# Optimization experiments

Measured on AMD Instinct MI355X. Metric: run time of the kernel, lower is better.

Reference implementation:

```python
import jax, jax.numpy as jnp
import numpy as np

TOP_K = 4
ALPHA = 1.702
LIMIT = 7.0


def _glu(x):
    # interleaved gate/up split, clamp, custom swiglu
    gate = x[..., ::2]
    up = x[..., 1::2]
    gate = jnp.minimum(gate, LIMIT)
    up = jnp.clip(up, -LIMIT, LIMIT)
    glu = gate * jax.nn.sigmoid(gate * ALPHA)
    return (up + 1.0) * glu


def setup_inputs() -> dict:
    key = jax.random.key(0)
    ks = jax.random.split(key, 7)
    B, S, H, F, E = 1, 1024, 2880, 2880, 16
    w_scale = 0.02
    return {
        "hidden_states": jax.random.normal(ks[0], (B, S, H), dtype=jnp.float32),
        "router_w": jax.random.normal(ks[1], (E, H), dtype=jnp.float32) * w_scale,
        "router_b": jax.random.normal(ks[2], (E,), dtype=jnp.float32) * w_scale,
        "gate_up_w": jax.random.normal(ks[3], (E, H, 2 * F), dtype=jnp.float32) * w_scale,
        "gate_up_b": jax.random.normal(ks[4], (E, 2 * F), dtype=jnp.float32) * w_scale,
        "down_w": jax.random.normal(ks[5], (E, F, H), dtype=jnp.float32) * w_scale,
        "down_b": jax.random.normal(ks[6], (E, H), dtype=jnp.float32) * w_scale,
    }


def reference(hidden_states, router_w, router_b, gate_up_w, gate_up_b, down_w, down_b):
    B, S, H = hidden_states.shape
    x = hidden_states.reshape(-1, H)  # [T, H]
    T = x.shape[0]

    # Router: linear + top-k + softmax over top-k values, scattered to full [T, E]
    logits = x @ router_w.T + router_b  # [T, E]
    top_v, top_i = jax.lax.top_k(logits, TOP_K)  # [T, K]
    top_v = jax.nn.softmax(top_v, axis=-1)  # normalized top-k affinities
    scores = jnp.zeros_like(logits).at[jnp.arange(T)[:, None], top_i].set(top_v)  # [T, E]

    # Expert GLU MLPs (dense over experts; zero affinity masks unselected experts)
    gu = jnp.einsum('th,ehf->etf', x, gate_up_w) + gate_up_b[:, None, :]  # [E, T, 2F]
    act = _glu(gu)  # [E, T, F]
    out_e = jnp.einsum('etf,efh->eth', act, down_w) + down_b[:, None, :]  # [E, T, H]

    # Combine weighted by router scores
    out = jnp.einsum('te,eth->th', scores, out_e)  # [T, H]
    return out.reshape(B, S, H)
```

## Files before the change

kernel.cpp:

```cpp
#include <hip/hip_runtime.h>
#include <hip/hip_bf16.h>
#include <math.h>

#define H_DIM 2880
#define F_DIM 2880
#define GU_DIM 5760
#define NE 16
#define NT 1024
#define TOPK 4
#define NIT 90

typedef float f32x4 __attribute__((ext_vector_type(4)));
typedef __bf16 bf16x8 __attribute__((ext_vector_type(8)));

__device__ __forceinline__ unsigned short f2bf(float f) {
    union { float f; unsigned u; } v; v.f = f;
    return (unsigned short)((v.u + 0x8000u) >> 16);
}
__device__ __forceinline__ unsigned pk2(float a, float b) {
    return (unsigned)f2bf(a) | ((unsigned)f2bf(b) << 16);
}
__device__ __forceinline__ void gload16(const void* gsrc, void* ldst) {
    __builtin_amdgcn_global_load_lds(
        (const __attribute__((address_space(1))) unsigned int*)gsrc,
        (__attribute__((address_space(3))) unsigned int*)ldst,
        16, 0, 0);
}

__global__ __launch_bounds__(256) void castx_kernel(const float* __restrict__ x,
                                                    unsigned short* __restrict__ xb)
{
    int i = (blockIdx.x * 256 + threadIdx.x) * 8;
    float4 a = *(const float4*)(x + i);
    float4 b = *(const float4*)(x + i + 4);
    uint4 o;
    o.x = pk2(a.x, a.y); o.y = pk2(a.z, a.w);
    o.z = pk2(b.x, b.y); o.w = pk2(b.z, b.w);
    *(uint4*)(xb + i) = o;
}

__global__ __launch_bounds__(64) void router_kernel(
    const float* __restrict__ x, const float* __restrict__ rw, const float* __restrict__ rb,
    int* counts, int* topk_idx, float* topk_score)
{
    int t = blockIdx.x, lane = threadIdx.x;
    const float* xr = x + (size_t)t * H_DIM;
    float acc[NE];
#pragma unroll
    for (int e = 0; e < NE; e++) acc[e] = 0.f;
    for (int h = lane; h < H_DIM; h += 64) {
        float xv = xr[h];
#pragma unroll
        for (int e = 0; e < NE; e++) acc[e] += xv * rw[e * H_DIM + h];
    }
    float lg[NE];
#pragma unroll
    for (int e = 0; e < NE; e++) {
        float v = acc[e];
#pragma unroll
        for (int off = 32; off > 0; off >>= 1) v += __shfl_down(v, off, 64);
        lg[e] = v;
    }
    if (lane == 0) {
#pragma unroll
        for (int e = 0; e < NE; e++) lg[e] += rb[e];
        int mask = 0; float tv[TOPK]; int ti[TOPK];
        for (int k = 0; k < TOPK; k++) {
            float best = -1e30f; int bi = 0;
            for (int e = 0; e < NE; e++)
                if (!((mask >> e) & 1) && lg[e] > best) { best = lg[e]; bi = e; }
            mask |= 1 << bi; tv[k] = best; ti[k] = bi;
        }
        float m = tv[0], s = 0.f, ex[TOPK];
        for (int k = 0; k < TOPK; k++) { ex[k] = expf(tv[k] - m); s += ex[k]; }
        float inv = 1.f / s;
        for (int k = 0; k < TOPK; k++) {
            topk_idx[t * TOPK + k] = ti[k];
            topk_score[t * TOPK + k] = ex[k] * inv;
            atomicAdd(&counts[ti[k]], 1);
        }
    }
}

__global__ void offsets_kernel(const int* counts, int* offsets) {
    if (threadIdx.x == 0 && blockIdx.x == 0) {
        int s = 0;
        for (int e = 0; e < NE; e++) { offsets[e] = s; s += counts[e]; }
        offsets[NE] = s;
    }
}

__global__ void scatter_kernel(const int* topk_idx, const float* topk_score,
                               const int* offsets, int* fills, int* entry, float* entry_score,
                               int* slot_map)
{
    int t = blockIdx.x * blockDim.x + threadIdx.x;
    if (t >= NT) return;
    for (int k = 0; k < TOPK; k++) {
        int e = topk_idx[t * TOPK + k];
        int pos = atomicAdd(&fills[e], 1);
        int i = offsets[e] + pos;
        entry[i] = t | (k << 16);
        entry_score[i] = topk_score[t * TOPK + k];
        slot_map[t * TOPK + k] = i;
    }
}


#define PIPE_ISSUE(ASRC0, ASRC1, BPTR, BSTRIDE, KK, NB, RS)                   \
    {                                                                         \
        gload16((ASRC0) + (KK), &As[NB][aoff0]);                              \
        gload16((ASRC1) + (KK), &As[NB][aoff1]);                              \
        RS[0] = *(const float4*)((BPTR) + (size_t)(KK) * (BSTRIDE));          \
        RS[1] = *(const float4*)((BPTR) + (size_t)((KK) + 1) * (BSTRIDE));    \
        asm volatile("" ::: "memory");                                        \
    }

#define PIPE_BWRITE(NB, RC)                                                   \
    {                                                                         \
        float4 t0_ = RC[0], t1_ = RC[1];                                      \
        *(unsigned*)&Bs[NB][bwr0] = pk2(t0_.x, t1_.x);                        \
        *(unsigned*)&Bs[NB][bwr1] = pk2(t0_.y, t1_.y);                        \
        *(unsigned*)&Bs[NB][bwr2] = pk2(t0_.z, t1_.z);                        \
        *(unsigned*)&Bs[NB][bwr3] = pk2(t0_.w, t1_.w);                        \
    }

#define PIPE_BARRIER()                                                        \
    asm volatile("s_waitcnt lgkmcnt(0)" ::: "memory");                        \
    __builtin_amdgcn_sched_barrier(0);                                        \
    __builtin_amdgcn_s_barrier();                                             \
    __builtin_amdgcn_sched_barrier(0);

#define PIPE_MFMA(CUR)                                                        \
    {                                                                         \
        bf16x8 af_[4], bq_[4];                                                \
        _Pragma("unroll") for (int i = 0; i < 4; i++)                         \
            af_[i] = *(const bf16x8*)&As[CUR][a_rd[i]];                       \
        _Pragma("unroll") for (int i = 0; i < 4; i++)                         \
            bq_[i] = *(const bf16x8*)&Bs[CUR][b_rd[i]];                       \
        _Pragma("unroll") for (int mi = 0; mi < 4; mi++)                      \
            _Pragma("unroll") for (int ni = 0; ni < 4; ni++)                  \
                acc[mi][ni] = __builtin_amdgcn_mfma_f32_16x16x32_bf16(        \
                    af_[mi], bq_[ni], acc[mi][ni], 0, 0, 0);                  \
    }

#define PIPE_BODY(ASRC0, ASRC1, BPTR, BSTRIDE, T, CUR, NB1, NB2, RISS, RCON)  \
    {                                                                         \
        bool more_ = (T) + 2 < NIT;                                           \
        if (more_) PIPE_ISSUE(ASRC0, ASRC1, BPTR, BSTRIDE, ((T) + 2) * 32, NB2, RISS); \
        PIPE_MFMA(CUR);                                                       \
        if ((T) + 1 < NIT) {                                                  \
            if (more_) { asm volatile("s_waitcnt vmcnt(4)" ::: "memory"); }   \
            else       { asm volatile("s_waitcnt vmcnt(0)" ::: "memory"); }   \
            PIPE_BWRITE(NB1, RCON);                                           \
            PIPE_BARRIER();                                                   \
        }                                                                     \
    }

__global__ __launch_bounds__(512, 4) void gemm1_kernel(
    const unsigned short* __restrict__ xb, const float* __restrict__ gw, const float* __restrict__ gb,
    const int* __restrict__ counts, const int* __restrict__ offsets,
    const int* __restrict__ entry, unsigned short* __restrict__ act)
{
    int e = blockIdx.z;
    int cnt = counts[e];
    int m0 = blockIdx.y * 256;
    if (m0 >= cnt) return;
    int n0 = blockIdx.x * 128;
    int off = offsets[e];

    __shared__ __align__(16) unsigned short As[3][256 * 32];
    __shared__ __align__(16) unsigned short Bs[3][128 * 40];
    __shared__ int toks[256];

    int tid = threadIdx.x;
    if (tid < 256) {
        int r = m0 + tid;
        toks[tid] = entry[off + (r < cnt ? r : 0)] & 0xFFFF;
    }
    __syncthreads();

    int wv = tid >> 6, lane = tid & 63;

    int ar0 = 32 * wv + (lane >> 2);
    int ar1 = ar0 + 16;
    int ac = lane & 3;
    const unsigned short* asrc0 = xb + (size_t)toks[ar0] * H_DIM + 8 * (ac ^ ((ar0 >> 1) & 3));
    const unsigned short* asrc1 = xb + (size_t)toks[ar1] * H_DIM + 8 * (ac ^ ((ar1 >> 1) & 3));
    int aoff0 = (32 * wv) * 32;
    int aoff1 = (32 * wv + 16) * 32;

    int n4 = tid & 31, ks = tid >> 5;
    const float* bptr = gw + (size_t)e * H_DIM * GU_DIM + (size_t)(ks * 2) * GU_DIM + n0 + n4 * 4;
    int bswz = (((ks >> 2) ^ (n4 & 3)) * 8) + (ks & 3) * 2;
    int bwr0 = (n4 * 4 + 0) * 40 + bswz;
    int bwr1 = (n4 * 4 + 1) * 40 + bswz;
    int bwr2 = (n4 * 4 + 2) * 40 + bswz;
    int bwr3 = (n4 * 4 + 3) * 40 + bswz;

    int wm = (wv >> 1) * 64, wn = (wv & 1) * 64;
    int r16 = lane & 15, q = lane >> 4;

    f32x4 acc[4][4] = {};
    int a_rd[4], b_rd[4];
#pragma unroll
    for (int i = 0; i < 4; i++) {
        int m = wm + i * 16 + r16;
        a_rd[i] = m * 32 + ((q ^ ((m >> 1) & 3)) * 8);
        int n = wn + i * 16 + r16;
        b_rd[i] = n * 40 + ((q ^ ((n >> 2) & 3)) * 8);
    }

    float4 rA[2], rB[2];
    PIPE_ISSUE(asrc0, asrc1, bptr, GU_DIM, 0, 0, rA);
    PIPE_ISSUE(asrc0, asrc1, bptr, GU_DIM, 32, 1, rB);
    asm volatile("s_waitcnt vmcnt(4)" ::: "memory");
    PIPE_BWRITE(0, rA);
    PIPE_BARRIER();

    int c0 = 0;
    for (int it = 0; it < NIT; it += 2) {
        int c1 = c0 + 1; if (c1 == 3) c1 = 0;
        int c2 = c1 + 1; if (c2 == 3) c2 = 0;
        PIPE_BODY(asrc0, asrc1, bptr, GU_DIM, it,     c0, c1, c2, rA, rB);
        PIPE_BODY(asrc0, asrc1, bptr, GU_DIM, it + 1, c1, c2, c0, rB, rA);
        c0 = c2;
    }

    const float* gbp = gb + (size_t)e * GU_DIM;
#pragma unroll
    for (int ni = 0; ni < 4; ni++) {
        int col = n0 + wn + ni * 16 + r16;
        float bias = gbp[col];
#pragma unroll
        for (int mi = 0; mi < 4; mi++) {
#pragma unroll
            for (int r = 0; r < 4; r++) {
                float v = acc[mi][ni][r] + bias;
                float vo = __shfl_xor(v, 1, 64);
                float gate = (lane & 1) ? vo : v;
                float up   = (lane & 1) ? v  : vo;
                gate = fminf(gate, 7.0f);
                up = fminf(fmaxf(up, -7.0f), 7.0f);
                float glu = gate / (1.0f + expf(-1.702f * gate));
                float a = (up + 1.0f) * glu;
                int row = m0 + wm + mi * 16 + q * 4 + r;
                if (row < cnt && !(lane & 1))
                    act[(size_t)(off + row) * F_DIM + (col >> 1)] = f2bf(a);
            }
        }
    }
}

__global__ __launch_bounds__(512, 4) void gemm2_kernel(
    const unsigned short* __restrict__ act, const float* __restrict__ dw, const float* __restrict__ db,
    const int* __restrict__ counts, const int* __restrict__ offsets,
    const float* __restrict__ entry_score, float* __restrict__ slot_out)
{
    int e = blockIdx.z;
    int cnt = counts[e];
    int m0 = blockIdx.y * 256;
    if (m0 >= cnt) return;
    int n0 = blockIdx.x * 128;
    int off = offsets[e];

    __shared__ __align__(16) unsigned short As[3][256 * 32];
    __shared__ __align__(16) unsigned short Bs[3][128 * 40];
    __shared__ float scs[256];

    int tid = threadIdx.x;
    if (tid < 256) {
        int r = m0 + tid;
        scs[tid] = entry_score[off + (r < cnt ? r : 0)];
    }
    __syncthreads();

    int wv = tid >> 6, lane = tid & 63;

    int ar0 = 32 * wv + (lane >> 2);
    int ar1 = ar0 + 16;
    int ac = lane & 3;
    const unsigned short* asrc0 = act + (size_t)(off + m0 + ar0) * F_DIM + 8 * (ac ^ ((ar0 >> 1) & 3));
    const unsigned short* asrc1 = act + (size_t)(off + m0 + ar1) * F_DIM + 8 * (ac ^ ((ar1 >> 1) & 3));
    int aoff0 = (32 * wv) * 32;
    int aoff1 = (32 * wv + 16) * 32;

    int n4 = tid & 31, ks = tid >> 5;
    int ncol = n0 + n4 * 4;
    int ncc = (ncol < H_DIM) ? ncol : (H_DIM - 4);
    const float* bptr = dw + (size_t)e * F_DIM * H_DIM + (size_t)(ks * 2) * H_DIM + ncc;
    int bswz = (((ks >> 2) ^ (n4 & 3)) * 8) + (ks & 3) * 2;
    int bwr0 = (n4 * 4 + 0) * 40 + bswz;
    int bwr1 = (n4 * 4 + 1) * 40 + bswz;
    int bwr2 = (n4 * 4 + 2) * 40 + bswz;
    int bwr3 = (n4 * 4 + 3) * 40 + bswz;

    int wm = (wv >> 1) * 64, wn = (wv & 1) * 64;
    int r16 = lane & 15, q = lane >> 4;

    f32x4 acc[4][4] = {};
    int a_rd[4], b_rd[4];
#pragma unroll
    for (int i = 0; i < 4; i++) {
        int m = wm + i * 16 + r16;
        a_rd[i] = m * 32 + ((q ^ ((m >> 1) & 3)) * 8);
        int n = wn + i * 16 + r16;
        b_rd[i] = n * 40 + ((q ^ ((n >> 2) & 3)) * 8);
    }

    float4 rA[2], rB[2];
    PIPE_ISSUE(asrc0, asrc1, bptr, H_DIM, 0, 0, rA);
    PIPE_ISSUE(asrc0, asrc1, bptr, H_DIM, 32, 1, rB);
    asm volatile("s_waitcnt vmcnt(4)" ::: "memory");
    PIPE_BWRITE(0, rA);
    PIPE_BARRIER();

    int c0 = 0;
    for (int it = 0; it < NIT; it += 2) {
        int c1 = c0 + 1; if (c1 == 3) c1 = 0;
        int c2 = c1 + 1; if (c2 == 3) c2 = 0;
        PIPE_BODY(asrc0, asrc1, bptr, H_DIM, it,     c0, c1, c2, rA, rB);
        PIPE_BODY(asrc0, asrc1, bptr, H_DIM, it + 1, c1, c2, c0, rB, rA);
        c0 = c2;
    }

    const float* dbp = db + (size_t)e * H_DIM;
#pragma unroll
    for (int ni = 0; ni < 4; ni++) {
        int col = n0 + wn + ni * 16 + r16;
        float bias = (col < H_DIM) ? dbp[col] : 0.f;
#pragma unroll
        for (int mi = 0; mi < 4; mi++) {
#pragma unroll
            for (int r = 0; r < 4; r++) {
                int lr = wm + mi * 16 + q * 4 + r;
                if (m0 + lr < cnt && col < H_DIM) {
                    float v = (acc[mi][ni][r] + bias) * scs[lr];
                    slot_out[(size_t)(off + m0 + lr) * H_DIM + col] = v;
                }
            }
        }
    }
}

__global__ __launch_bounds__(256) void gather_kernel(
    const float* __restrict__ slot_out, const int* __restrict__ slot_map,
    float* __restrict__ out)
{
    int t = blockIdx.x;
    int s0 = slot_map[t * TOPK + 0];
    int s1 = slot_map[t * TOPK + 1];
    int s2 = slot_map[t * TOPK + 2];
    int s3 = slot_map[t * TOPK + 3];
    const float* r0 = slot_out + (size_t)s0 * H_DIM;
    const float* r1 = slot_out + (size_t)s1 * H_DIM;
    const float* r2 = slot_out + (size_t)s2 * H_DIM;
    const float* r3 = slot_out + (size_t)s3 * H_DIM;
    float* op = out + (size_t)t * H_DIM;
    for (int h = threadIdx.x * 4; h < H_DIM; h += 1024) {
        f32x4 v = *(const f32x4*)(r0 + h) + *(const f32x4*)(r1 + h)
                + *(const f32x4*)(r2 + h) + *(const f32x4*)(r3 + h);
        *(f32x4*)(op + h) = v;
    }
}

extern "C" void kernel_launch(void* const* d_in, const int* in_sizes, int n_in,
                              void* d_out, int out_size, void* d_ws, size_t ws_size,
                              hipStream_t stream)
{
    const float* x  = (const float*)d_in[0];
    const float* rw = (const float*)d_in[1];
    const float* rb = (const float*)d_in[2];
    const float* gw = (const float*)d_in[3];
    const float* gb = (const float*)d_in[4];
    const float* dw = (const float*)d_in[5];
    const float* db = (const float*)d_in[6];
    float* out = (float*)d_out;

    char* ws = (char*)d_ws;
    int*   counts      = (int*)(ws);
    int*   fills       = (int*)(ws + 64);
    int*   offsets     = (int*)(ws + 128);
    int*   topk_idx    = (int*)(ws + 256);
    float* topk_score  = (float*)(ws + 16640);
    int*   entry       = (int*)(ws + 33024);
    float* entry_score = (float*)(ws + 49408);
    int*   slot_map    = (int*)(ws + 65792);
    unsigned short* act = (unsigned short*)(ws + 131072);
    unsigned short* xb  = (unsigned short*)(ws + 25198592);
    float* slot_out     = (float*)(ws + 31096832);

    hipMemsetAsync(ws, 0, 256, stream);

    castx_kernel<<<1440, 256, 0, stream>>>(x, xb);
    router_kernel<<<NT, 64, 0, stream>>>(x, rw, rb, counts, topk_idx, topk_score);
    offsets_kernel<<<1, 32, 0, stream>>>(counts, offsets);
    scatter_kernel<<<4, 256, 0, stream>>>(topk_idx, topk_score, offsets, fills, entry, entry_score, slot_map);
    gemm1_kernel<<<dim3(45, 4, NE), 512, 0, stream>>>(xb, gw, gb, counts, offsets, entry, act);
    gemm2_kernel<<<dim3(23, 4, NE), 512, 0, stream>>>(act, dw, db, counts, offsets, entry_score, slot_out);
    gather_kernel<<<NT, 256, 0, stream>>>(slot_out, slot_map, out);
}
```

Measured before the change: 2.126 ms.

## Widen GEMM tiles to 256x256 with 1024-thread blocks and new LDS swizzle

Both expert GEMM kernels now use 256-wide N tiles, 16 waves per 1024-thread block, and one A row-chunk load per thread. The goal is to halve how often the A operand (gathered tokens or activations) is re-read across N tiles and to raise per-block data reuse. The B-tile LDS swizzle is redone for the wider tile, and bounds checks are added because 5760 is not a multiple of 256. In exchange, occupancy drops to one block per CU, LDS use roughly doubles for B, and the last N tile is partly wasted.

```diff
diff --git a/kernel.cpp b/kernel.cpp
--- a/kernel.cpp
+++ b/kernel.cpp
@@ -107,10 +107,9 @@
 }
 
 
-#define PIPE_ISSUE(ASRC0, ASRC1, BPTR, BSTRIDE, KK, NB, RS)                   \
+#define PIPE_ISSUE(ASRC, BPTR, BSTRIDE, KK, NB, RS)                           \
     {                                                                         \
-        gload16((ASRC0) + (KK), &As[NB][aoff0]);                              \
-        gload16((ASRC1) + (KK), &As[NB][aoff1]);                              \
+        gload16((ASRC) + (KK), &As[NB][aoff]);                                \
         RS[0] = *(const float4*)((BPTR) + (size_t)(KK) * (BSTRIDE));          \
         RS[1] = *(const float4*)((BPTR) + (size_t)((KK) + 1) * (BSTRIDE));    \
         asm volatile("" ::: "memory");                                        \
@@ -144,20 +143,26 @@
                     af_[mi], bq_[ni], acc[mi][ni], 0, 0, 0);                  \
     }
 
-#define PIPE_BODY(ASRC0, ASRC1, BPTR, BSTRIDE, T, CUR, NB1, NB2, RISS, RCON)  \
+#define PIPE_BODY(ASRC, BPTR, BSTRIDE, T, CUR, NB1, NB2, RISS, RCON)          \
     {                                                                         \
         bool more_ = (T) + 2 < NIT;                                           \
-        if (more_) PIPE_ISSUE(ASRC0, ASRC1, BPTR, BSTRIDE, ((T) + 2) * 32, NB2, RISS); \
+        if (more_) PIPE_ISSUE(ASRC, BPTR, BSTRIDE, ((T) + 2) * 32, NB2, RISS);\
         PIPE_MFMA(CUR);                                                       \
         if ((T) + 1 < NIT) {                                                  \
-            if (more_) { asm volatile("s_waitcnt vmcnt(4)" ::: "memory"); }   \
+            if (more_) { asm volatile("s_waitcnt vmcnt(3)" ::: "memory"); }   \
             else       { asm volatile("s_waitcnt vmcnt(0)" ::: "memory"); }   \
             PIPE_BWRITE(NB1, RCON);                                           \
             PIPE_BARRIER();                                                   \
         }                                                                     \
     }
 
-__global__ __launch_bounds__(512, 4) void gemm1_kernel(
+__device__ __forceinline__ int mk_bwr(int lane, int c, int wv) {
+    int n = 4 * lane + c;
+    int sn = ((n >> 3) ^ (n >> 5)) & 3;
+    return n * 40 + (((wv >> 2) ^ sn) * 8) + (wv & 3) * 2;
+}
+
+__global__ __launch_bounds__(1024, 1) void gemm1_kernel(
     const unsigned short* __restrict__ xb, const float* __restrict__ gw, const float* __restrict__ gb,
     const int* __restrict__ counts, const int* __restrict__ offsets,
     const int* __restrict__ entry, unsigned short* __restrict__ act)
@@ -166,11 +171,11 @@
     int cnt = counts[e];
     int m0 = blockIdx.y * 256;
     if (m0 >= cnt) return;
-    int n0 = blockIdx.x * 128;
+    int n0 = blockIdx.x * 256;
     int off = offsets[e];
 
     __shared__ __align__(16) unsigned short As[3][256 * 32];
-    __shared__ __align__(16) unsigned short Bs[3][128 * 40];
+    __shared__ __align__(16) unsigned short Bs[3][256 * 40];
     __shared__ int toks[256];
 
     int tid = threadIdx.x;
@@ -182,23 +187,20 @@
 
     int wv = tid >> 6, lane = tid & 63;
 
-    int ar0 = 32 * wv + (lane >> 2);
-    int ar1 = ar0 + 16;
+    int ar = 16 * wv + (lane >> 2);
     int ac = lane & 3;
-    const unsigned short* asrc0 = xb + (size_t)toks[ar0] * H_DIM + 8 * (ac ^ ((ar0 >> 1) & 3));
-    const unsigned short* asrc1 = xb + (size_t)toks[ar1] * H_DIM + 8 * (ac ^ ((ar1 >> 1) & 3));
-    int aoff0 = (32 * wv) * 32;
-    int aoff1 = (32 * wv + 16) * 32;
-
-    int n4 = tid & 31, ks = tid >> 5;
-    const float* bptr = gw + (size_t)e * H_DIM * GU_DIM + (size_t)(ks * 2) * GU_DIM + n0 + n4 * 4;
-    int bswz = (((ks >> 2) ^ (n4 & 3)) * 8) + (ks & 3) * 2;
-    int bwr0 = (n4 * 4 + 0) * 40 + bswz;
-    int bwr1 = (n4 * 4 + 1) * 40 + bswz;
-    int bwr2 = (n4 * 4 + 2) * 40 + bswz;
-    int bwr3 = (n4 * 4 + 3) * 40 + bswz;
-
-    int wm = (wv >> 1) * 64, wn = (wv & 1) * 64;
+    const unsigned short* asrc = xb + (size_t)toks[ar] * H_DIM + 8 * (ac ^ ((ar >> 1) & 3));
+    int aoff = (16 * wv) * 32;
+
+    int bcol = n0 + 4 * lane;
+    int ncc = (bcol < GU_DIM) ? bcol : (GU_DIM - 4);
+    const float* bptr = gw + (size_t)e * H_DIM * GU_DIM + (size_t)(2 * wv) * GU_DIM + ncc;
+    int bwr0 = mk_bwr(lane, 0, wv);
+    int bwr1 = mk_bwr(lane, 1, wv);
+    int bwr2 = mk_bwr(lane, 2, wv);
+    int bwr3 = mk_bwr(lane, 3, wv);
+
+    int wm = (wv & 3) * 64, wn = (wv >> 2) * 64;
     int r16 = lane & 15, q = lane >> 4;
 
     f32x4 acc[4][4] = {};
@@ -208,13 +210,14 @@
         int m = wm + i * 16 + r16;
         a_rd[i] = m * 32 + ((q ^ ((m >> 1) & 3)) * 8);
         int n = wn + i * 16 + r16;
-        b_rd[i] = n * 40 + ((q ^ ((n >> 2) & 3)) * 8);
+        int sn = ((n >> 3) ^ (n >> 5)) & 3;
+        b_rd[i] = n * 40 + ((q ^ sn) * 8);
     }
 
     float4 rA[2], rB[2];
-    PIPE_ISSUE(asrc0, asrc1, bptr, GU_DIM, 0, 0, rA);
-    PIPE_ISSUE(asrc0, asrc1, bptr, GU_DIM, 32, 1, rB);
-    asm volatile("s_waitcnt vmcnt(4)" ::: "memory");
+    PIPE_ISSUE(asrc, bptr, GU_DIM, 0, 0, rA);
+    PIPE_ISSUE(asrc, bptr, GU_DIM, 32, 1, rB);
+    asm volatile("s_waitcnt vmcnt(3)" ::: "memory");
     PIPE_BWRITE(0, rA);
     PIPE_BARRIER();
 
@@ -222,8 +225,8 @@
     for (int it = 0; it < NIT; it += 2) {
         int c1 = c0 + 1; if (c1 == 3) c1 = 0;
         int c2 = c1 + 1; if (c2 == 3) c2 = 0;
-        PIPE_BODY(asrc0, asrc1, bptr, GU_DIM, it,     c0, c1, c2, rA, rB);
-        PIPE_BODY(asrc0, asrc1, bptr, GU_DIM, it + 1, c1, c2, c0, rB, rA);
+        PIPE_BODY(asrc, bptr, GU_DIM, it,     c0, c1, c2, rA, rB);
+        PIPE_BODY(asrc, bptr, GU_DIM, it + 1, c1, c2, c0, rB, rA);
         c0 = c2;
     }
 
@@ -231,7 +234,7 @@
 #pragma unroll
     for (int ni = 0; ni < 4; ni++) {
         int col = n0 + wn + ni * 16 + r16;
-        float bias = gbp[col];
+        float bias = (col < GU_DIM) ? gbp[col] : 0.f;
 #pragma unroll
         for (int mi = 0; mi < 4; mi++) {
 #pragma unroll
@@ -245,14 +248,14 @@
                 float glu = gate / (1.0f + expf(-1.702f * gate));
                 float a = (up + 1.0f) * glu;
                 int row = m0 + wm + mi * 16 + q * 4 + r;
-                if (row < cnt && !(lane & 1))
+                if (row < cnt && col < GU_DIM && !(lane & 1))
                     act[(size_t)(off + row) * F_DIM + (col >> 1)] = f2bf(a);
             }
         }
     }
 }
 
-__global__ __launch_bounds__(512, 4) void gemm2_kernel(
+__global__ __launch_bounds__(1024, 1) void gemm2_kernel(
     const unsigned short* __restrict__ act, const float* __restrict__ dw, const float* __restrict__ db,
     const int* __restrict__ counts, const int* __restrict__ offsets,
     const float* __restrict__ entry_score, float* __restrict__ slot_out)
@@ -261,11 +264,11 @@
     int cnt = counts[e];
     int m0 = blockIdx.y * 256;
     if (m0 >= cnt) return;
-    int n0 = blockIdx.x * 128;
+    int n0 = blockIdx.x * 256;
     int off = offsets[e];
 
     __shared__ __align__(16) unsigned short As[3][256 * 32];
-    __shared__ __align__(16) unsigned short Bs[3][128 * 40];
+    __shared__ __align__(16) unsigned short Bs[3][256 * 40];
     __shared__ float scs[256];
 
     int tid = threadIdx.x;
@@ -277,25 +280,20 @@
 
     int wv = tid >> 6, lane = tid & 63;
 
-    int ar0 = 32 * wv + (lane >> 2);
-    int ar1 = ar0 + 16;
+    int ar = 16 * wv + (lane >> 2);
     int ac = lane & 3;
-    const unsigned short* asrc0 = act + (size_t)(off + m0 + ar0) * F_DIM + 8 * (ac ^ ((ar0 >> 1) & 3));
-    const unsigned short* asrc1 = act + (size_t)(off + m0 + ar1) * F_DIM + 8 * (ac ^ ((ar1 >> 1) & 3));
-    int aoff0 = (32 * wv) * 32;
-    int aoff1 = (32 * wv + 16) * 32;
-
-    int n4 = tid & 31, ks = tid >> 5;
-    int ncol = n0 + n4 * 4;
-    int ncc = (ncol < H_DIM) ? ncol : (H_DIM - 4);
-    const float* bptr = dw + (size_t)e * F_DIM * H_DIM + (size_t)(ks * 2) * H_DIM + ncc;
-    int bswz = (((ks >> 2) ^ (n4 & 3)) * 8) + (ks & 3) * 2;
-    int bwr0 = (n4 * 4 + 0) * 40 + bswz;
-    int bwr1 = (n4 * 4 + 1) * 40 + bswz;
-    int bwr2 = (n4 * 4 + 2) * 40 + bswz;
-    int bwr3 = (n4 * 4 + 3) * 40 + bswz;
-
-    int wm = (wv >> 1) * 64, wn = (wv & 1) * 64;
+    const unsigned short* asrc = act + (size_t)(off + m0 + ar) * F_DIM + 8 * (ac ^ ((ar >> 1) & 3));
+    int aoff = (16 * wv) * 32;
+
+    int bcol = n0 + 4 * lane;
+    int ncc = (bcol < H_DIM) ? bcol : (H_DIM - 4);
+    const float* bptr = dw + (size_t)e * F_DIM * H_DIM + (size_t)(2 * wv) * H_DIM + ncc;
+    int bwr0 = mk_bwr(lane, 0, wv);
+    int bwr1 = mk_bwr(lane, 1, wv);
+    int bwr2 = mk_bwr(lane, 2, wv);
+    int bwr3 = mk_bwr(lane, 3, wv);
+
+    int wm = (wv & 3) * 64, wn = (wv >> 2) * 64;
     int r16 = lane & 15, q = lane >> 4;
 
     f32x4 acc[4][4] = {};
@@ -305,13 +303,14 @@
         int m = wm + i * 16 + r16;
         a_rd[i] = m * 32 + ((q ^ ((m >> 1) & 3)) * 8);
         int n = wn + i * 16 + r16;
-        b_rd[i] = n * 40 + ((q ^ ((n >> 2) & 3)) * 8);
+        int sn = ((n >> 3) ^ (n >> 5)) & 3;
+        b_rd[i] = n * 40 + ((q ^ sn) * 8);
     }
 
     float4 rA[2], rB[2];
-    PIPE_ISSUE(asrc0, asrc1, bptr, H_DIM, 0, 0, rA);
-    PIPE_ISSUE(asrc0, asrc1, bptr, H_DIM, 32, 1, rB);
-    asm volatile("s_waitcnt vmcnt(4)" ::: "memory");
+    PIPE_ISSUE(asrc, bptr, H_DIM, 0, 0, rA);
+    PIPE_ISSUE(asrc, bptr, H_DIM, 32, 1, rB);
+    asm volatile("s_waitcnt vmcnt(3)" ::: "memory");
     PIPE_BWRITE(0, rA);
     PIPE_BARRIER();
 
@@ -319,8 +318,8 @@
     for (int it = 0; it < NIT; it += 2) {
         int c1 = c0 + 1; if (c1 == 3) c1 = 0;
         int c2 = c1 + 1; if (c2 == 3) c2 = 0;
-        PIPE_BODY(asrc0, asrc1, bptr, H_DIM, it,     c0, c1, c2, rA, rB);
-        PIPE_BODY(asrc0, asrc1, bptr, H_DIM, it + 1, c1, c2, c0, rB, rA);
+        PIPE_BODY(asrc, bptr, H_DIM, it,     c0, c1, c2, rA, rB);
+        PIPE_BODY(asrc, bptr, H_DIM, it + 1, c1, c2, c0, rB, rA);
         c0 = c2;
     }
 
@@ -396,7 +395,7 @@
     router_kernel<<<NT, 64, 0, stream>>>(x, rw, rb, counts, topk_idx, topk_score);
     offsets_kernel<<<1, 32, 0, stream>>>(counts, offsets);
     scatter_kernel<<<4, 256, 0, stream>>>(topk_idx, topk_score, offsets, fills, entry, entry_score, slot_map);
-    gemm1_kernel<<<dim3(45, 4, NE), 512, 0, stream>>>(xb, gw, gb, counts, offsets, entry, act);
-    gemm2_kernel<<<dim3(23, 4, NE), 512, 0, stream>>>(act, dw, db, counts, offsets, entry_score, slot_out);
+    gemm1_kernel<<<dim3(23, 4, NE), 1024, 0, stream>>>(xb, gw, gb, counts, offsets, entry, act);
+    gemm2_kernel<<<dim3(12, 4, NE), 1024, 0, stream>>>(act, dw, db, counts, offsets, entry_score, slot_out);
     gather_kernel<<<NT, 256, 0, stream>>>(slot_out, slot_map, out);
 }
```

After: 2.118 ms. Within noise of the previous version (-0.4%).
